# Kernel optimization log

Hardware: AMD Instinct MI355X
Metric: run time of the kernel (lower is better)

Reference implementation:

```python
import jax, jax.numpy as jnp
import numpy as np

B, S, OBS, NINS, H, NBLK = 1024, 512, 5, 2, 32, 4
EPS = 1e-6


def setup_inputs() -> dict:
    key = jax.random.key(0)
    ks = jax.random.split(key, 10)
    obs_sequence = jax.random.normal(ks[0], (B, S, OBS), jnp.float32)
    prev_actions = jax.random.normal(ks[1], (B, S, NINS), jnp.float32)
    fan_in = OBS + NINS
    # xavier-uniform input projection
    lim_in = np.sqrt(6.0 / (fan_in + H))
    W_in = jax.random.uniform(ks[2], (H, fan_in), jnp.float32, -lim_in, lim_in)
    b_in = jnp.zeros((H,), jnp.float32)
    rms_w = jnp.ones((NBLK, H), jnp.float32)
    # LSTMCell default init: U(-1/sqrt(H), 1/sqrt(H)); gate order i,f,g,o
    s = 1.0 / np.sqrt(H)
    W_ih = jax.random.uniform(ks[3], (NBLK, 4 * H, H), jnp.float32, -s, s)
    W_hh = jax.random.uniform(ks[4], (NBLK, 4 * H, H), jnp.float32, -s, s)
    b_ih = jax.random.uniform(ks[5], (NBLK, 4 * H), jnp.float32, -s, s)
    b_hh = jax.random.uniform(ks[6], (NBLK, 4 * H), jnp.float32, -s, s)
    # heads: kaiming-uniform (linear, fan_in) scaled by 1e-3, zero bias
    lim_h = np.sqrt(3.0 / H)
    head_w = jax.random.uniform(ks[7], (NINS, H), jnp.float32, -lim_h, lim_h) * 1e-3
    head_b = jnp.zeros((NINS,), jnp.float32)
    return dict(obs_sequence=obs_sequence, prev_actions=prev_actions,
                W_in=W_in, b_in=b_in, rms_w=rms_w,
                W_ih=W_ih, W_hh=W_hh, b_ih=b_ih, b_hh=b_hh,
                head_w=head_w, head_b=head_b)


def reference(obs_sequence, prev_actions, W_in, b_in, rms_w,
              W_ih, W_hh, b_ih, b_hh, head_w, head_b):
    batch = obs_sequence.shape[0]
    hdim = W_in.shape[0]
    x = jnp.concatenate([obs_sequence, prev_actions], axis=-1) @ W_in.T + b_in  # [B,S,H]
    xs = jnp.swapaxes(x, 0, 1)  # [S,B,H] for scan over time
    h0 = jnp.zeros((NBLK, batch, hdim), x.dtype)
    c0 = jnp.zeros((NBLK, batch, hdim), x.dtype)

    def step(carry, xt):
        h, c = carry
        hs, cs = [], []
        for k in range(NBLK):  # small fixed stack of distinct blocks
            rms = jnp.sqrt(jnp.mean(xt * xt, axis=-1, keepdims=True) + EPS)
            xn = rms_w[k] * (xt / rms)
            gates = xn @ W_ih[k].T + b_ih[k] + h[k] @ W_hh[k].T + b_hh[k]  # [B,4H]
            i, f, g, o = jnp.split(gates, 4, axis=-1)
            c_new = jax.nn.sigmoid(f) * c[k] + jax.nn.sigmoid(i) * jnp.tanh(g)
            h_new = jax.nn.sigmoid(o) * jnp.tanh(c_new)
            xt = xt + h_new  # residual
            hs.append(h_new)
            cs.append(c_new)
        return (jnp.stack(hs), jnp.stack(cs)), xt

    (hT, cT), ys = jax.lax.scan(step, (h0, c0), xs)  # ys: [S,B,H]
    raw = jnp.einsum('sbh,ih->ibs', ys, head_w) + head_b[:, None, None]  # [NINS,B,S]
    out = jnp.sign(raw) * (jnp.exp(jnp.abs(raw)) - 1.0)  # symexp
    lim = jnp.array([5.0, 10.0], out.dtype)[:, None, None]
    out = jnp.clip(out, -lim, lim)
    return out, hT, cT
```

## Files before the change

kernel.cpp:

```cpp
#include <hip/hip_runtime.h>


constexpr int B_ = 1024, S_ = 512, OBS_ = 5, NINS_ = 2, H_ = 32, NBLK_ = 4;
constexpr int SUP_ = 4;
constexpr int TT_ = S_ / SUP_;
constexpr float EPS_ = 1e-6f;
constexpr float LOG2E_ = 1.4426950408889634f;

typedef __fp16 h2 __attribute__((ext_vector_type(2)));
typedef __fp16 h8 __attribute__((ext_vector_type(8)));
typedef float  f4 __attribute__((ext_vector_type(4)));
typedef int    i4 __attribute__((ext_vector_type(4)));

__device__ __forceinline__ float rcp_(float x) { return __builtin_amdgcn_rcpf(x); }
__device__ __forceinline__ float rsq_(float x) { return __builtin_amdgcn_rsqf(x); }
__device__ __forceinline__ float ex2_(float x) { return __builtin_amdgcn_exp2f(x); }
__device__ __forceinline__ h2 pk_(float a, float b) {
  return __builtin_amdgcn_cvt_pkrtz(a, b);
}
__device__ __forceinline__ h8 pk8_(f4 lo, f4 hi) {
  i4 q;
  q[0] = __builtin_bit_cast(int, pk_(lo[0], lo[1]));
  q[1] = __builtin_bit_cast(int, pk_(lo[2], lo[3]));
  q[2] = __builtin_bit_cast(int, pk_(hi[0], hi[1]));
  q[3] = __builtin_bit_cast(int, pk_(hi[2], hi[3]));
  return __builtin_bit_cast(h8, q);
}
__device__ __forceinline__ f4 mfma_(h8 a, h8 b, f4 c) {
  return __builtin_amdgcn_mfma_f32_16x16x32_f16(a, b, c, 0, 0, 0);
}
__device__ __forceinline__ f4 e4n_(f4 a) {
  f4 r;
  r[0] = ex2_(-a[0]); r[1] = ex2_(-a[1]);
  r[2] = ex2_(-a[2]); r[3] = ex2_(-a[3]);
  return r;
}
__device__ __forceinline__ f4 rcp4_(f4 a) {
  f4 r;
  r[0] = rcp_(a[0]); r[1] = rcp_(a[1]);
  r[2] = rcp_(a[2]); r[3] = rcp_(a[3]);
  return r;
}
__device__ __forceinline__ float dot44_(f4 a, f4 x, f4 b2, f4 y) {
  float s = a[0] * x[0];
  s = fmaf(a[1], x[1], s); s = fmaf(a[2], x[2], s); s = fmaf(a[3], x[3], s);
  s = fmaf(b2[0], y[0], s); s = fmaf(b2[1], y[1], s);
  s = fmaf(b2[2], y[2], s); s = fmaf(b2[3], y[3], s);
  return s;
}
__device__ __forceinline__ float psw16_(float v, bool re) {
#if __has_builtin(__builtin_amdgcn_permlane16_swap)
  auto r = __builtin_amdgcn_permlane16_swap(
      __builtin_bit_cast(int, v), __builtin_bit_cast(int, v), false, false);
  return __builtin_bit_cast(float, re ? (int)r[1] : (int)r[0]);
#else
  return __shfl_xor(v, 16);
#endif
}
__device__ __forceinline__ float psw32_(float v, bool lo) {
#if __has_builtin(__builtin_amdgcn_permlane32_swap)
  auto r = __builtin_amdgcn_permlane32_swap(
      __builtin_bit_cast(int, v), __builtin_bit_cast(int, v), false, false);
  return __builtin_bit_cast(float, lo ? (int)r[1] : (int)r[0]);
#else
  return __shfl_xor(v, 32);
#endif
}

#define ACT_TILE(GI, GF, GG, GO, C, HV) do {                               \
    const f4 _one = {1.f, 1.f, 1.f, 1.f};                                  \
    const f4 _Ei = e4n_(GI);                                               \
    const f4 _Eg = e4n_(GG);                                               \
    const f4 _Ef = e4n_(GF);                                               \
    const f4 _sitg = (_one - _Eg) * rcp4_((_one + _Ei) * (_one + _Eg));    \
    const f4 _sf = rcp4_(_one + _Ef);                                      \
    (C) = _sf * (C) + _sitg;                                               \
    const f4 _Eo = e4n_(GO);                                               \
    const f4 _Ec = e4n_((C) * (2.f * LOG2E_));                             \
    (HV) = (_one - _Ec) * rcp4_((_one + _Eo) * (_one + _Ec));              \
  } while (0)

__global__ __launch_bounds__(256, 1) void garch_mfma7_kernel(
    const float* __restrict__ obs, const float* __restrict__ prev,
    const float* __restrict__ W_in, const float* __restrict__ b_in,
    const float* __restrict__ rms_w,
    const float* __restrict__ W_ih, const float* __restrict__ W_hh,
    const float* __restrict__ b_ih, const float* __restrict__ b_hh,
    const float* __restrict__ head_w, const float* __restrict__ head_b,
    float* __restrict__ out) {
  const int tid  = threadIdx.x;
  const int k    = tid >> 6;
  const int lane = tid & 63;
  const int g    = lane >> 4;
  const int b    = lane & 15;
  const int bg   = blockIdx.x * 16 + b;
  const bool re_ = ((lane >> 4) & 1) == 0;
  const bool lo_ = (lane < 32);

  __shared__ __align__(16) float xslot[3][2][SUP_][16][36];

  h8 wx[8], wh[8];
  f4 biasv[8];
  {
    const size_t wb = (size_t)k * 128 * 32;
#pragma unroll
    for (int mi = 0; mi < 8; ++mi) {
      const float scl = (mi == 4 || mi == 5) ? 2.f * LOG2E_ : LOG2E_;
      const int row = 16 * mi + b;
      const float* px = W_ih + wb + (size_t)row * 32;
      f4 x0 = *(const f4*)(px + 4 * g);
      f4 x1 = *(const f4*)(px + 16 + 4 * g);
      wx[mi] = pk8_(x0 * scl, x1 * scl);
      const float* ph = W_hh + wb + (size_t)row * 32;
      f4 h0v = *(const f4*)(ph + 4 * g);
      f4 h1v = *(const f4*)(ph + 16 + 4 * g);
      wh[mi] = pk8_(h0v * scl, h1v * scl);
      f4 bv;
#pragma unroll
      for (int r = 0; r < 4; ++r) {
        const int gr = k * 128 + 16 * mi + 4 * g + r;
        bv[r] = (b_ih[gr] + b_hh[gr]) * scl;
      }
      biasv[mi] = bv;
    }
  }
  f4 rw0v, rw1v;
#pragma unroll
  for (int r = 0; r < 4; ++r) {
    rw0v[r] = rms_w[k * 32 + 4 * g + r];
    rw1v[r] = rms_w[k * 32 + 16 + 4 * g + r];
  }

  h8 winA0 = {}, winA1 = {};
  f4 bin0v = {}, bin1v = {};
  const float* obs_b = nullptr; const float* prev_b = nullptr;
  f4 cin[SUP_] = {}, nin[SUP_] = {};
  if (k == 0) {
    f4 lo0, lo1; const f4 z = {};
#pragma unroll
    for (int r = 0; r < 4; ++r) {
      const int kk = 4 * g + r;
      lo0[r] = (kk < 7) ? W_in[(size_t)b * 7 + kk] : 0.f;
      lo1[r] = (kk < 7) ? W_in[(size_t)(16 + b) * 7 + kk] : 0.f;
    }
    winA0 = pk8_(lo0, z);
    winA1 = pk8_(lo1, z);
#pragma unroll
    for (int r = 0; r < 4; ++r) {
      bin0v[r] = b_in[4 * g + r];
      bin1v[r] = b_in[16 + 4 * g + r];
    }
    obs_b  = obs  + (size_t)bg * S_ * OBS_;
    prev_b = prev + (size_t)bg * S_ * NINS_;
#pragma unroll
    for (int s = 0; s < SUP_; ++s) {
      const float* o = obs_b + (size_t)s * OBS_;
      if (g == 0)      { cin[s][0] = o[0]; cin[s][1] = o[1]; cin[s][2] = o[2]; cin[s][3] = o[3]; }
      else if (g == 1) { cin[s][0] = o[4]; cin[s][1] = prev_b[2 * s]; cin[s][2] = prev_b[2 * s + 1]; cin[s][3] = 0.f; }
    }
  }
  f4 hw00 = {}, hw01 = {}, hw10 = {}, hw11 = {};
  float hb0 = 0.f, hb1 = 0.f;
  if (k == 3) {
#pragma unroll
    for (int r = 0; r < 4; ++r) {
      hw00[r] = head_w[4 * g + r]      * LOG2E_;
      hw01[r] = head_w[16 + 4 * g + r] * LOG2E_;
      hw10[r] = head_w[32 + 4 * g + r] * LOG2E_;
      hw11[r] = head_w[48 + 4 * g + r] * LOG2E_;
    }
    hb0 = head_b[0] * LOG2E_;
    hb1 = head_b[1] * LOG2E_;
  }

  f4 c0 = {}, c1 = {}, hv0 = {}, hv1 = {};

  float* out_y  = out;
  float* out_hT = out + (size_t)NINS_ * B_ * S_;
  float* out_cT = out_hT + (size_t)NBLK_ * B_ * H_;

  for (int tau = 0; tau < TT_ + NBLK_ - 1; ++tau) {
    __syncthreads();
    const int tt = tau - k;
    if (tt < 0 || tt >= TT_) continue;
    const int t0 = SUP_ * tt;
    const int wp = tau & 1, rp = (tau + 1) & 1;

    f4 x0[SUP_], x1[SUP_];
    if (k == 0) {
      if (tt + 1 < TT_) {
#pragma unroll
        for (int s = 0; s < SUP_; ++s) {
          const int t = t0 + SUP_ + s;
          const float* o = obs_b + (size_t)t * OBS_;
          if (g == 0)      { nin[s][0] = o[0]; nin[s][1] = o[1]; nin[s][2] = o[2]; nin[s][3] = o[3]; }
          else if (g == 1) { nin[s][0] = o[4]; nin[s][1] = prev_b[2 * t]; nin[s][2] = prev_b[2 * t + 1]; nin[s][3] = 0.f; }
        }
      }
      const f4 z = {};
#pragma unroll
      for (int s = 0; s < SUP_; ++s) {
        const h8 binp = pk8_(cin[s], z);
        x0[s] = mfma_(winA0, binp, bin0v);
        x1[s] = mfma_(winA1, binp, bin1v);
      }
    } else {
#pragma unroll
      for (int s = 0; s < SUP_; ++s) {
        x0[s] = *(const f4*)&xslot[k - 1][rp][s][b][4 * g];
        x1[s] = *(const f4*)&xslot[k - 1][rp][s][b][16 + 4 * g];
      }
    }

    h8 bx[SUP_];
#pragma unroll
    for (int s = 0; s < SUP_; ++s) {
      float ss = dot44_(x0[s], x0[s], x1[s], x1[s]);
      ss += psw16_(ss, re_);
      ss += psw32_(ss, lo_);
      const float rinv = rsq_(ss * (1.0f / 32.0f) + EPS_);
      bx[s] = pk8_(x0[s] * (rw0v * rinv), x1[s] * (rw1v * rinv));
    }
    f4 gx[SUP_][8];
#pragma unroll
    for (int s = 0; s < SUP_; ++s) {
#pragma unroll
      for (int m = 0; m < 8; ++m) {
        gx[s][m] = mfma_(wx[m], bx[s], biasv[m]);
      }
    }

#pragma unroll
    for (int s = 0; s < SUP_; ++s) {
      const h8 bh = pk8_(hv0, hv1);
      const f4 gi0 = mfma_(wh[0], bh, gx[s][0]);
      const f4 gi1 = mfma_(wh[1], bh, gx[s][1]);
      const f4 gf0 = mfma_(wh[2], bh, gx[s][2]);
      const f4 gf1 = mfma_(wh[3], bh, gx[s][3]);
      const f4 gg0 = mfma_(wh[4], bh, gx[s][4]);
      const f4 gg1 = mfma_(wh[5], bh, gx[s][5]);
      const f4 go0 = mfma_(wh[6], bh, gx[s][6]);
      const f4 go1 = mfma_(wh[7], bh, gx[s][7]);
      ACT_TILE(gi0, gf0, gg0, go0, c0, hv0);
      ACT_TILE(gi1, gf1, gg1, go1, c1, hv1);
      x0[s] += hv0;
      x1[s] += hv1;
    }

    if (k < 3) {
#pragma unroll
      for (int s = 0; s < SUP_; ++s) {
        *(f4*)&xslot[k][wp][s][b][4 * g]      = x0[s];
        *(f4*)&xslot[k][wp][s][b][16 + 4 * g] = x1[s];
      }
    } else {
      float p0[SUP_], p1[SUP_];
#pragma unroll
      for (int s = 0; s < SUP_; ++s) {
        float a = dot44_(hw00, x0[s], hw01, x1[s]);
        float bq = dot44_(hw10, x0[s], hw11, x1[s]);
        a += psw16_(a, re_); a += psw32_(a, lo_);
        bq += psw16_(bq, re_); bq += psw32_(bq, lo_);
        p0[s] = a + hb0;
        p1[s] = bq + hb1;
      }
      if (lane < 16) {
        f4 v0, v1;
#pragma unroll
        for (int s = 0; s < SUP_; ++s) {
          v0[s] = copysignf(fminf(ex2_(fabsf(p0[s])) - 1.f, 5.f),  p0[s]);
          v1[s] = copysignf(fminf(ex2_(fabsf(p1[s])) - 1.f, 10.f), p1[s]);
        }
        *(f4*)&out_y[(size_t)bg * S_ + t0]                   = v0;
        *(f4*)&out_y[(size_t)B_ * S_ + (size_t)bg * S_ + t0] = v1;
      }
    }

    if (tt == TT_ - 1) {
      float* hp = out_hT + ((size_t)k * B_ + bg) * H_;
      float* cp = out_cT + ((size_t)k * B_ + bg) * H_;
#pragma unroll
      for (int r = 0; r < 4; ++r) {
        hp[4 * g + r]      = hv0[r];
        hp[16 + 4 * g + r] = hv1[r];
        cp[4 * g + r]      = c0[r];
        cp[16 + 4 * g + r] = c1[r];
      }
    }

    if (k == 0) {
#pragma unroll
      for (int s = 0; s < SUP_; ++s) cin[s] = nin[s];
    }
  }
}

extern "C" void kernel_launch(void* const* d_in, const int* in_sizes, int n_in,
                              void* d_out, int out_size, void* d_ws, size_t ws_size,
                              hipStream_t stream) {
  (void)in_sizes; (void)n_in; (void)d_ws; (void)ws_size; (void)out_size;
  garch_mfma7_kernel<<<dim3(B_ / 16), dim3(256), 0, stream>>>(
      (const float*)d_in[0],
      (const float*)d_in[1],
      (const float*)d_in[2],
      (const float*)d_in[3],
      (const float*)d_in[4],
      (const float*)d_in[5],
      (const float*)d_in[6],
      (const float*)d_in[7],
      (const float*)d_in[8],
      (const float*)d_in[9],
      (const float*)d_in[10],
      (float*)d_out);
}
```

Before: 429.4 us.

## Double timesteps per barrier stage and merge LSTM sigmoid reciprocals

```diff
diff --git a/kernel.cpp b/kernel.cpp
--- a/kernel.cpp
+++ b/kernel.cpp
@@ -2,7 +2,8 @@
 
 
 constexpr int B_ = 1024, S_ = 512, OBS_ = 5, NINS_ = 2, H_ = 32, NBLK_ = 4;
-constexpr int SUP_ = 4;
+constexpr int SUP_ = 8;
+constexpr int PH_  = 4;
 constexpr int TT_ = S_ / SUP_;
 constexpr float EPS_ = 1e-6f;
 constexpr float LOG2E_ = 1.4426950408889634f;
@@ -72,15 +73,18 @@
     const f4 _Ei = e4n_(GI);                                               \
     const f4 _Eg = e4n_(GG);                                               \
     const f4 _Ef = e4n_(GF);                                               \
-    const f4 _sitg = (_one - _Eg) * rcp4_((_one + _Ei) * (_one + _Eg));    \
-    const f4 _sf = rcp4_(_one + _Ef);                                      \
+    const f4 _a = (_one + _Ei) * (_one + _Eg);                             \
+    const f4 _f = _one + _Ef;                                              \
+    const f4 _r = rcp4_(_a * _f);                                          \
+    const f4 _sitg = (_one - _Eg) * _f * _r;                               \
+    const f4 _sf = _a * _r;                                                \
     (C) = _sf * (C) + _sitg;                                               \
     const f4 _Eo = e4n_(GO);                                               \
     const f4 _Ec = e4n_((C) * (2.f * LOG2E_));                             \
     (HV) = (_one - _Ec) * rcp4_((_one + _Eo) * (_one + _Ec));              \
   } while (0)
 
-__global__ __launch_bounds__(256, 1) void garch_mfma7_kernel(
+__global__ __launch_bounds__(256, 1) void garch_mfma8_kernel(
     const float* __restrict__ obs, const float* __restrict__ prev,
     const float* __restrict__ W_in, const float* __restrict__ b_in,
     const float* __restrict__ rms_w,
@@ -134,7 +138,7 @@
   h8 winA0 = {}, winA1 = {};
   f4 bin0v = {}, bin1v = {};
   const float* obs_b = nullptr; const float* prev_b = nullptr;
-  f4 cin[SUP_] = {}, nin[SUP_] = {};
+  f4 cin[SUP_] = {};
   if (k == 0) {
     f4 lo0, lo1; const f4 z = {};
 #pragma unroll
@@ -186,93 +190,100 @@
     const int t0 = SUP_ * tt;
     const int wp = tau & 1, rp = (tau + 1) & 1;
 
-    f4 x0[SUP_], x1[SUP_];
-    if (k == 0) {
-      if (tt + 1 < TT_) {
-#pragma unroll
-        for (int s = 0; s < SUP_; ++s) {
-          const int t = t0 + SUP_ + s;
-          const float* o = obs_b + (size_t)t * OBS_;
-          if (g == 0)      { nin[s][0] = o[0]; nin[s][1] = o[1]; nin[s][2] = o[2]; nin[s][3] = o[3]; }
-          else if (g == 1) { nin[s][0] = o[4]; nin[s][1] = prev_b[2 * t]; nin[s][2] = prev_b[2 * t + 1]; nin[s][3] = 0.f; }
-        }
-      }
-      const f4 z = {};
-#pragma unroll
-      for (int s = 0; s < SUP_; ++s) {
-        const h8 binp = pk8_(cin[s], z);
-        x0[s] = mfma_(winA0, binp, bin0v);
-        x1[s] = mfma_(winA1, binp, bin1v);
-      }
-    } else {
-#pragma unroll
-      for (int s = 0; s < SUP_; ++s) {
-        x0[s] = *(const f4*)&xslot[k - 1][rp][s][b][4 * g];
-        x1[s] = *(const f4*)&xslot[k - 1][rp][s][b][16 + 4 * g];
-      }
-    }
-
-    h8 bx[SUP_];
-#pragma unroll
-    for (int s = 0; s < SUP_; ++s) {
-      float ss = dot44_(x0[s], x0[s], x1[s], x1[s]);
-      ss += psw16_(ss, re_);
-      ss += psw32_(ss, lo_);
-      const float rinv = rsq_(ss * (1.0f / 32.0f) + EPS_);
-      bx[s] = pk8_(x0[s] * (rw0v * rinv), x1[s] * (rw1v * rinv));
-    }
-    f4 gx[SUP_][8];
-#pragma unroll
-    for (int s = 0; s < SUP_; ++s) {
-#pragma unroll
-      for (int m = 0; m < 8; ++m) {
-        gx[s][m] = mfma_(wx[m], bx[s], biasv[m]);
-      }
-    }
-
-#pragma unroll
-    for (int s = 0; s < SUP_; ++s) {
-      const h8 bh = pk8_(hv0, hv1);
-      const f4 gi0 = mfma_(wh[0], bh, gx[s][0]);
-      const f4 gi1 = mfma_(wh[1], bh, gx[s][1]);
-      const f4 gf0 = mfma_(wh[2], bh, gx[s][2]);
-      const f4 gf1 = mfma_(wh[3], bh, gx[s][3]);
-      const f4 gg0 = mfma_(wh[4], bh, gx[s][4]);
-      const f4 gg1 = mfma_(wh[5], bh, gx[s][5]);
-      const f4 go0 = mfma_(wh[6], bh, gx[s][6]);
-      const f4 go1 = mfma_(wh[7], bh, gx[s][7]);
-      ACT_TILE(gi0, gf0, gg0, go0, c0, hv0);
-      ACT_TILE(gi1, gf1, gg1, go1, c1, hv1);
-      x0[s] += hv0;
-      x1[s] += hv1;
-    }
-
-    if (k < 3) {
-#pragma unroll
-      for (int s = 0; s < SUP_; ++s) {
-        *(f4*)&xslot[k][wp][s][b][4 * g]      = x0[s];
-        *(f4*)&xslot[k][wp][s][b][16 + 4 * g] = x1[s];
-      }
-    } else {
-      float p0[SUP_], p1[SUP_];
-#pragma unroll
-      for (int s = 0; s < SUP_; ++s) {
-        float a = dot44_(hw00, x0[s], hw01, x1[s]);
-        float bq = dot44_(hw10, x0[s], hw11, x1[s]);
-        a += psw16_(a, re_); a += psw32_(a, lo_);
-        bq += psw16_(bq, re_); bq += psw32_(bq, lo_);
-        p0[s] = a + hb0;
-        p1[s] = bq + hb1;
-      }
-      if (lane < 16) {
-        f4 v0, v1;
-#pragma unroll
-        for (int s = 0; s < SUP_; ++s) {
-          v0[s] = copysignf(fminf(ex2_(fabsf(p0[s])) - 1.f, 5.f),  p0[s]);
-          v1[s] = copysignf(fminf(ex2_(fabsf(p1[s])) - 1.f, 10.f), p1[s]);
-        }
-        *(f4*)&out_y[(size_t)bg * S_ + t0]                   = v0;
-        *(f4*)&out_y[(size_t)B_ * S_ + (size_t)bg * S_ + t0] = v1;
+#pragma unroll
+    for (int p = 0; p < SUP_ / PH_; ++p) {
+      f4 x0[PH_], x1[PH_];
+      if (k == 0) {
+        const f4 z = {};
+#pragma unroll
+        for (int s = 0; s < PH_; ++s) {
+          const int sg_ = p * PH_ + s;
+          const h8 binp = pk8_(cin[sg_], z);
+          x0[s] = mfma_(winA0, binp, bin0v);
+          x1[s] = mfma_(winA1, binp, bin1v);
+        }
+        if (tt + 1 < TT_) {
+#pragma unroll
+          for (int s = 0; s < PH_; ++s) {
+            const int sg_ = p * PH_ + s;
+            const int t = t0 + SUP_ + sg_;
+            const float* o = obs_b + (size_t)t * OBS_;
+            if (g == 0)      { cin[sg_][0] = o[0]; cin[sg_][1] = o[1]; cin[sg_][2] = o[2]; cin[sg_][3] = o[3]; }
+            else if (g == 1) { cin[sg_][0] = o[4]; cin[sg_][1] = prev_b[2 * t]; cin[sg_][2] = prev_b[2 * t + 1]; cin[sg_][3] = 0.f; }
+          }
+        }
+      } else {
+#pragma unroll
+        for (int s = 0; s < PH_; ++s) {
+          const int sg_ = p * PH_ + s;
+          x0[s] = *(const f4*)&xslot[k - 1][rp][sg_][b][4 * g];
+          x1[s] = *(const f4*)&xslot[k - 1][rp][sg_][b][16 + 4 * g];
+        }
+      }
+
+      h8 bx[PH_];
+#pragma unroll
+      for (int s = 0; s < PH_; ++s) {
+        float ss = dot44_(x0[s], x0[s], x1[s], x1[s]);
+        ss += psw16_(ss, re_);
+        ss += psw32_(ss, lo_);
+        const float rinv = rsq_(ss * (1.0f / 32.0f) + EPS_);
+        bx[s] = pk8_(x0[s] * (rw0v * rinv), x1[s] * (rw1v * rinv));
+      }
+      f4 gx[PH_][8];
+#pragma unroll
+      for (int s = 0; s < PH_; ++s) {
+#pragma unroll
+        for (int m = 0; m < 8; ++m) {
+          gx[s][m] = mfma_(wx[m], bx[s], biasv[m]);
+        }
+      }
+
+#pragma unroll
+      for (int s = 0; s < PH_; ++s) {
+        const h8 bh = pk8_(hv0, hv1);
+        const f4 gi0 = mfma_(wh[0], bh, gx[s][0]);
+        const f4 gi1 = mfma_(wh[1], bh, gx[s][1]);
+        const f4 gf0 = mfma_(wh[2], bh, gx[s][2]);
+        const f4 gf1 = mfma_(wh[3], bh, gx[s][3]);
+        const f4 gg0 = mfma_(wh[4], bh, gx[s][4]);
+        const f4 gg1 = mfma_(wh[5], bh, gx[s][5]);
+        const f4 go0 = mfma_(wh[6], bh, gx[s][6]);
+        const f4 go1 = mfma_(wh[7], bh, gx[s][7]);
+        ACT_TILE(gi0, gf0, gg0, go0, c0, hv0);
+        ACT_TILE(gi1, gf1, gg1, go1, c1, hv1);
+        x0[s] += hv0;
+        x1[s] += hv1;
+      }
+
+      if (k < 3) {
+#pragma unroll
+        for (int s = 0; s < PH_; ++s) {
+          const int sg_ = p * PH_ + s;
+          *(f4*)&xslot[k][wp][sg_][b][4 * g]      = x0[s];
+          *(f4*)&xslot[k][wp][sg_][b][16 + 4 * g] = x1[s];
+        }
+      } else {
+        float p0[PH_], p1[PH_];
+#pragma unroll
+        for (int s = 0; s < PH_; ++s) {
+          float a = dot44_(hw00, x0[s], hw01, x1[s]);
+          float bq = dot44_(hw10, x0[s], hw11, x1[s]);
+          a += psw16_(a, re_); a += psw32_(a, lo_);
+          bq += psw16_(bq, re_); bq += psw32_(bq, lo_);
+          p0[s] = a + hb0;
+          p1[s] = bq + hb1;
+        }
+        if (lane < 16) {
+          f4 v0, v1;
+#pragma unroll
+          for (int s = 0; s < PH_; ++s) {
+            v0[s] = copysignf(fminf(ex2_(fabsf(p0[s])) - 1.f, 5.f),  p0[s]);
+            v1[s] = copysignf(fminf(ex2_(fabsf(p1[s])) - 1.f, 10.f), p1[s]);
+          }
+          *(f4*)&out_y[(size_t)bg * S_ + t0 + p * PH_]                   = v0;
+          *(f4*)&out_y[(size_t)B_ * S_ + (size_t)bg * S_ + t0 + p * PH_] = v1;
+        }
       }
     }
 
@@ -287,11 +298,6 @@
         cp[16 + 4 * g + r] = c1[r];
       }
     }
-
-    if (k == 0) {
-#pragma unroll
-      for (int s = 0; s < SUP_; ++s) cin[s] = nin[s];
-    }
   }
 }
 
@@ -299,7 +305,7 @@
                               void* d_out, int out_size, void* d_ws, size_t ws_size,
                               hipStream_t stream) {
   (void)in_sizes; (void)n_in; (void)d_ws; (void)ws_size; (void)out_size;
-  garch_mfma7_kernel<<<dim3(B_ / 16), dim3(256), 0, stream>>>(
+  garch_mfma8_kernel<<<dim3(B_ / 16), dim3(256), 0, stream>>>(
       (const float*)d_in[0],
       (const float*)d_in[1],
       (const float*)d_in[2],
```

Result: no change. 425.7 us, median of 2 (-0.9%).

## Split each LSTM block across two waves with LDS flag handoff per step

Applied to the files above, without the earlier changes.

```diff
diff --git a/kernel.cpp b/kernel.cpp
--- a/kernel.cpp
+++ b/kernel.cpp
@@ -41,11 +41,11 @@
   r[2] = rcp_(a[2]); r[3] = rcp_(a[3]);
   return r;
 }
-__device__ __forceinline__ float dot44_(f4 a, f4 x, f4 b2, f4 y) {
+__device__ __forceinline__ float dot4_(f4 a, f4 x) {
   float s = a[0] * x[0];
-  s = fmaf(a[1], x[1], s); s = fmaf(a[2], x[2], s); s = fmaf(a[3], x[3], s);
-  s = fmaf(b2[0], y[0], s); s = fmaf(b2[1], y[1], s);
-  s = fmaf(b2[2], y[2], s); s = fmaf(b2[3], y[3], s);
+  s = fmaf(a[1], x[1], s);
+  s = fmaf(a[2], x[2], s);
+  s = fmaf(a[3], x[3], s);
   return s;
 }
 __device__ __forceinline__ float psw16_(float v, bool re) {
@@ -66,21 +66,32 @@
   return __shfl_xor(v, 32);
 #endif
 }
-
-#define ACT_TILE(GI, GF, GG, GO, C, HV) do {                               \
+__device__ __forceinline__ void flag_st_(int* p, int v) {
+  __threadfence_block();
+  __hip_atomic_store(p, v, __ATOMIC_RELAXED, __HIP_MEMORY_SCOPE_WORKGROUP);
+}
+__device__ __forceinline__ void flag_wait_(int* p, int v) {
+  while (__hip_atomic_load(p, __ATOMIC_RELAXED, __HIP_MEMORY_SCOPE_WORKGROUP) < v) {}
+  __threadfence_block();
+}
+
+#define ACT1(GI, GF, GG, GO) do {                                          \
     const f4 _one = {1.f, 1.f, 1.f, 1.f};                                  \
     const f4 _Ei = e4n_(GI);                                               \
     const f4 _Eg = e4n_(GG);                                               \
     const f4 _Ef = e4n_(GF);                                               \
-    const f4 _sitg = (_one - _Eg) * rcp4_((_one + _Ei) * (_one + _Eg));    \
-    const f4 _sf = rcp4_(_one + _Ef);                                      \
-    (C) = _sf * (C) + _sitg;                                               \
+    const f4 _a = (_one + _Ei) * (_one + _Eg);                             \
+    const f4 _f = _one + _Ef;                                              \
+    const f4 _r = rcp4_(_a * _f);                                          \
+    const f4 _sitg = (_one - _Eg) * _f * _r;                               \
+    const f4 _sf = _a * _r;                                                \
+    c_own = _sf * c_own + _sitg;                                           \
     const f4 _Eo = e4n_(GO);                                               \
-    const f4 _Ec = e4n_((C) * (2.f * LOG2E_));                             \
-    (HV) = (_one - _Ec) * rcp4_((_one + _Eo) * (_one + _Ec));              \
+    const f4 _Ec = e4n_(c_own * (2.f * LOG2E_));                           \
+    hv_own = (_one - _Ec) * rcp4_((_one + _Eo) * (_one + _Ec));            \
   } while (0)
 
-__global__ __launch_bounds__(256, 1) void garch_mfma7_kernel(
+__global__ __launch_bounds__(512, 1) void garch_msplit2_kernel(
     const float* __restrict__ obs, const float* __restrict__ prev,
     const float* __restrict__ W_in, const float* __restrict__ b_in,
     const float* __restrict__ rms_w,
@@ -89,7 +100,9 @@
     const float* __restrict__ head_w, const float* __restrict__ head_b,
     float* __restrict__ out) {
   const int tid  = threadIdx.x;
-  const int k    = tid >> 6;
+  const int w    = tid >> 6;
+  const int k    = w & 3;
+  const int hf   = w >> 2;
   const int lane = tid & 63;
   const int g    = lane >> 4;
   const int b    = lane & 15;
@@ -98,58 +111,62 @@
   const bool lo_ = (lane < 32);
 
   __shared__ __align__(16) float xslot[3][2][SUP_][16][36];
-
-  h8 wx[8], wh[8];
-  f4 biasv[8];
+  __shared__ int   xnbuf[4][2][SUP_][64][2];
+  __shared__ int   hvbuf[4][2][2][64][2];
+  __shared__ float ssbuf[4][2][SUP_][16];
+  __shared__ float headbuf[2][SUP_][16];
+  __shared__ int   xnflag[4][2];
+  __shared__ int   hvflag[4][2];
+  __shared__ int   headflag;
+
+  for (int i = tid; i < 4 * 2 * 2 * 64 * 2; i += 512) ((int*)hvbuf)[i] = 0;
+  if (tid < 8) { xnflag[tid >> 1][tid & 1] = 0; hvflag[tid >> 1][tid & 1] = 0; }
+  if (tid == 8) headflag = 0;
+
+  h8 wx[4], wh[4];
+  f4 biasv[4];
   {
     const size_t wb = (size_t)k * 128 * 32;
 #pragma unroll
-    for (int mi = 0; mi < 8; ++mi) {
-      const float scl = (mi == 4 || mi == 5) ? 2.f * LOG2E_ : LOG2E_;
-      const int row = 16 * mi + b;
+    for (int l = 0; l < 4; ++l) {
+      const int m = 2 * l + hf;
+      const float scl = (l == 2) ? 2.f * LOG2E_ : LOG2E_;
+      const int row = 16 * m + b;
       const float* px = W_ih + wb + (size_t)row * 32;
       f4 x0 = *(const f4*)(px + 4 * g);
       f4 x1 = *(const f4*)(px + 16 + 4 * g);
-      wx[mi] = pk8_(x0 * scl, x1 * scl);
+      wx[l] = pk8_(x0 * scl, x1 * scl);
       const float* ph = W_hh + wb + (size_t)row * 32;
       f4 h0v = *(const f4*)(ph + 4 * g);
       f4 h1v = *(const f4*)(ph + 16 + 4 * g);
-      wh[mi] = pk8_(h0v * scl, h1v * scl);
+      wh[l] = pk8_(h0v * scl, h1v * scl);
       f4 bv;
 #pragma unroll
       for (int r = 0; r < 4; ++r) {
-        const int gr = k * 128 + 16 * mi + 4 * g + r;
+        const int gr = k * 128 + 16 * m + 4 * g + r;
         bv[r] = (b_ih[gr] + b_hh[gr]) * scl;
       }
-      biasv[mi] = bv;
+      biasv[l] = bv;
     }
   }
-  f4 rw0v, rw1v;
-#pragma unroll
-  for (int r = 0; r < 4; ++r) {
-    rw0v[r] = rms_w[k * 32 + 4 * g + r];
-    rw1v[r] = rms_w[k * 32 + 16 + 4 * g + r];
-  }
-
-  h8 winA0 = {}, winA1 = {};
-  f4 bin0v = {}, bin1v = {};
+  f4 rwv;
+#pragma unroll
+  for (int r = 0; r < 4; ++r) rwv[r] = rms_w[k * 32 + 16 * hf + 4 * g + r];
+
+  h8 win = {};
+  f4 binv = {};
   const float* obs_b = nullptr; const float* prev_b = nullptr;
   f4 cin[SUP_] = {}, nin[SUP_] = {};
   if (k == 0) {
-    f4 lo0, lo1; const f4 z = {};
+    f4 lw; const f4 z = {};
 #pragma unroll
     for (int r = 0; r < 4; ++r) {
       const int kk = 4 * g + r;
-      lo0[r] = (kk < 7) ? W_in[(size_t)b * 7 + kk] : 0.f;
-      lo1[r] = (kk < 7) ? W_in[(size_t)(16 + b) * 7 + kk] : 0.f;
-    }
-    winA0 = pk8_(lo0, z);
-    winA1 = pk8_(lo1, z);
-#pragma unroll
-    for (int r = 0; r < 4; ++r) {
-      bin0v[r] = b_in[4 * g + r];
-      bin1v[r] = b_in[16 + 4 * g + r];
-    }
+      lw[r] = (kk < 7) ? W_in[(size_t)(16 * hf + b) * 7 + kk] : 0.f;
+    }
+    win = pk8_(lw, z);
+#pragma unroll
+    for (int r = 0; r < 4; ++r) binv[r] = b_in[16 * hf + 4 * g + r];
     obs_b  = obs  + (size_t)bg * S_ * OBS_;
     prev_b = prev + (size_t)bg * S_ * NINS_;
 #pragma unroll
@@ -159,21 +176,20 @@
       else if (g == 1) { cin[s][0] = o[4]; cin[s][1] = prev_b[2 * s]; cin[s][2] = prev_b[2 * s + 1]; cin[s][3] = 0.f; }
     }
   }
-  f4 hw00 = {}, hw01 = {}, hw10 = {}, hw11 = {};
+  f4 hwa = {}, hwb = {};
   float hb0 = 0.f, hb1 = 0.f;
   if (k == 3) {
 #pragma unroll
     for (int r = 0; r < 4; ++r) {
-      hw00[r] = head_w[4 * g + r]      * LOG2E_;
-      hw01[r] = head_w[16 + 4 * g + r] * LOG2E_;
-      hw10[r] = head_w[32 + 4 * g + r] * LOG2E_;
-      hw11[r] = head_w[48 + 4 * g + r] * LOG2E_;
+      hwa[r] = head_w[16 * hf + 4 * g + r]      * LOG2E_;
+      hwb[r] = head_w[32 + 16 * hf + 4 * g + r] * LOG2E_;
     }
     hb0 = head_b[0] * LOG2E_;
     hb1 = head_b[1] * LOG2E_;
   }
 
-  f4 c0 = {}, c1 = {}, hv0 = {}, hv1 = {};
+  f4 c_own = {}, hv_own = {};
+  int hvpk0 = 0, hvpk1 = 0;
 
   float* out_y  = out;
   float* out_hT = out + (size_t)NINS_ * B_ * S_;
@@ -186,7 +202,7 @@
     const int t0 = SUP_ * tt;
     const int wp = tau & 1, rp = (tau + 1) & 1;
 
-    f4 x0[SUP_], x1[SUP_];
+    f4 xt[SUP_];
     if (k == 0) {
       if (tt + 1 < TT_) {
 #pragma unroll
@@ -201,78 +217,113 @@
 #pragma unroll
       for (int s = 0; s < SUP_; ++s) {
         const h8 binp = pk8_(cin[s], z);
-        x0[s] = mfma_(winA0, binp, bin0v);
-        x1[s] = mfma_(winA1, binp, bin1v);
+        xt[s] = mfma_(win, binp, binv);
       }
     } else {
 #pragma unroll
-      for (int s = 0; s < SUP_; ++s) {
-        x0[s] = *(const f4*)&xslot[k - 1][rp][s][b][4 * g];
-        x1[s] = *(const f4*)&xslot[k - 1][rp][s][b][16 + 4 * g];
-      }
-    }
-
-    h8 bx[SUP_];
-#pragma unroll
-    for (int s = 0; s < SUP_; ++s) {
-      float ss = dot44_(x0[s], x0[s], x1[s], x1[s]);
+      for (int s = 0; s < SUP_; ++s)
+        xt[s] = *(const f4*)&xslot[k - 1][rp][s][b][16 * hf + 4 * g];
+    }
+
+    int xnp0[SUP_], xnp1[SUP_];
+    float ssp[SUP_];
+#pragma unroll
+    for (int s = 0; s < SUP_; ++s) {
+      const f4 xn = xt[s] * rwv;
+      xnp0[s] = __builtin_bit_cast(int, pk_(xn[0], xn[1]));
+      xnp1[s] = __builtin_bit_cast(int, pk_(xn[2], xn[3]));
+      float ss = dot4_(xt[s], xt[s]);
       ss += psw16_(ss, re_);
       ss += psw32_(ss, lo_);
-      const float rinv = rsq_(ss * (1.0f / 32.0f) + EPS_);
-      bx[s] = pk8_(x0[s] * (rw0v * rinv), x1[s] * (rw1v * rinv));
-    }
-    f4 gx[SUP_][8];
-#pragma unroll
-    for (int s = 0; s < SUP_; ++s) {
-#pragma unroll
-      for (int m = 0; m < 8; ++m) {
-        gx[s][m] = mfma_(wx[m], bx[s], biasv[m]);
-      }
-    }
-
-#pragma unroll
-    for (int s = 0; s < SUP_; ++s) {
-      const h8 bh = pk8_(hv0, hv1);
-      const f4 gi0 = mfma_(wh[0], bh, gx[s][0]);
-      const f4 gi1 = mfma_(wh[1], bh, gx[s][1]);
-      const f4 gf0 = mfma_(wh[2], bh, gx[s][2]);
-      const f4 gf1 = mfma_(wh[3], bh, gx[s][3]);
-      const f4 gg0 = mfma_(wh[4], bh, gx[s][4]);
-      const f4 gg1 = mfma_(wh[5], bh, gx[s][5]);
-      const f4 go0 = mfma_(wh[6], bh, gx[s][6]);
-      const f4 go1 = mfma_(wh[7], bh, gx[s][7]);
-      ACT_TILE(gi0, gf0, gg0, go0, c0, hv0);
-      ACT_TILE(gi1, gf1, gg1, go1, c1, hv1);
-      x0[s] += hv0;
-      x1[s] += hv1;
+      ssp[s] = ss;
+      int* p = &xnbuf[k][hf][s][lane][0];
+      p[0] = xnp0[s]; p[1] = xnp1[s];
+      if (lane < 16) ssbuf[k][hf][s][lane] = ss;
+    }
+    flag_st_(&xnflag[k][hf], tt + 1);
+    flag_wait_(&xnflag[k][hf ^ 1], tt + 1);
+
+    float rinv[SUP_];
+    h8 bx[SUP_];
+#pragma unroll
+    for (int s = 0; s < SUP_; ++s) {
+      const int* p = &xnbuf[k][hf ^ 1][s][lane][0];
+      const int o0 = p[0], o1 = p[1];
+      i4 q;
+      if (hf == 0) { q[0] = xnp0[s]; q[1] = xnp1[s]; q[2] = o0; q[3] = o1; }
+      else         { q[0] = o0; q[1] = o1; q[2] = xnp0[s]; q[3] = xnp1[s]; }
+      bx[s] = __builtin_bit_cast(h8, q);
+      const float ss = ssp[s] + ssbuf[k][hf ^ 1][s][b];
+      rinv[s] = rsq_(ss * (1.0f / 32.0f) + EPS_);
+    }
+    f4 gx[SUP_][4];
+    const f4 z4 = {};
+#pragma unroll
+    for (int s = 0; s < SUP_; ++s) {
+#pragma unroll
+      for (int l = 0; l < 4; ++l) gx[s][l] = mfma_(wx[l], bx[s], z4);
+    }
+
+#pragma unroll
+    for (int s = 0; s < SUP_; ++s) {
+      const int gs = tt * SUP_ + s + 1;
+      flag_wait_(&hvflag[k][hf ^ 1], gs - 1);
+      const int* hp = &hvbuf[k][hf ^ 1][(gs - 1) & 1][lane][0];
+      const int ho0 = hp[0], ho1 = hp[1];
+      i4 qh;
+      if (hf == 0) { qh[0] = hvpk0; qh[1] = hvpk1; qh[2] = ho0; qh[3] = ho1; }
+      else         { qh[0] = ho0; qh[1] = ho1; qh[2] = hvpk0; qh[3] = hvpk1; }
+      const h8 bh = __builtin_bit_cast(h8, qh);
+      const f4 g0 = gx[s][0] * rinv[s] + mfma_(wh[0], bh, biasv[0]);
+      const f4 g1 = gx[s][1] * rinv[s] + mfma_(wh[1], bh, biasv[1]);
+      const f4 g2 = gx[s][2] * rinv[s] + mfma_(wh[2], bh, biasv[2]);
+      const f4 g3 = gx[s][3] * rinv[s] + mfma_(wh[3], bh, biasv[3]);
+      ACT1(g0, g1, g2, g3);
+      xt[s] += hv_own;
+      hvpk0 = __builtin_bit_cast(int, pk_(hv_own[0], hv_own[1]));
+      hvpk1 = __builtin_bit_cast(int, pk_(hv_own[2], hv_own[3]));
+      int* hq = &hvbuf[k][hf][gs & 1][lane][0];
+      hq[0] = hvpk0; hq[1] = hvpk1;
+      flag_st_(&hvflag[k][hf], gs);
     }
 
     if (k < 3) {
 #pragma unroll
+      for (int s = 0; s < SUP_; ++s)
+        *(f4*)&xslot[k][wp][s][b][16 * hf + 4 * g] = xt[s];
+    } else {
+      float pa[SUP_], pb[SUP_];
+#pragma unroll
       for (int s = 0; s < SUP_; ++s) {
-        *(f4*)&xslot[k][wp][s][b][4 * g]      = x0[s];
-        *(f4*)&xslot[k][wp][s][b][16 + 4 * g] = x1[s];
-      }
-    } else {
-      float p0[SUP_], p1[SUP_];
-#pragma unroll
-      for (int s = 0; s < SUP_; ++s) {
-        float a = dot44_(hw00, x0[s], hw01, x1[s]);
-        float bq = dot44_(hw10, x0[s], hw11, x1[s]);
-        a += psw16_(a, re_); a += psw32_(a, lo_);
-        bq += psw16_(bq, re_); bq += psw32_(bq, lo_);
-        p0[s] = a + hb0;
-        p1[s] = bq + hb1;
-      }
-      if (lane < 16) {
-        f4 v0, v1;
-#pragma unroll
-        for (int s = 0; s < SUP_; ++s) {
-          v0[s] = copysignf(fminf(ex2_(fabsf(p0[s])) - 1.f, 5.f),  p0[s]);
-          v1[s] = copysignf(fminf(ex2_(fabsf(p1[s])) - 1.f, 10.f), p1[s]);
+        float a = dot4_(hwa, xt[s]);
+        float bb = dot4_(hwb, xt[s]);
+        a += psw16_(a, re_);  a += psw32_(a, lo_);
+        bb += psw16_(bb, re_); bb += psw32_(bb, lo_);
+        pa[s] = a; pb[s] = bb;
+      }
+      if (hf == 0) {
+        if (lane < 16) {
+#pragma unroll
+          for (int s = 0; s < SUP_; ++s) {
+            headbuf[0][s][lane] = pa[s];
+            headbuf[1][s][lane] = pb[s];
+          }
         }
-        *(f4*)&out_y[(size_t)bg * S_ + t0]                   = v0;
-        *(f4*)&out_y[(size_t)B_ * S_ + (size_t)bg * S_ + t0] = v1;
+        flag_st_(&headflag, tt + 1);
+      } else {
+        flag_wait_(&headflag, tt + 1);
+        if (lane < 16) {
+          f4 v0, v1;
+#pragma unroll
+          for (int s = 0; s < SUP_; ++s) {
+            const float p0 = pa[s] + headbuf[0][s][lane] + hb0;
+            const float p1 = pb[s] + headbuf[1][s][lane] + hb1;
+            v0[s] = copysignf(fminf(ex2_(fabsf(p0)) - 1.f, 5.f),  p0);
+            v1[s] = copysignf(fminf(ex2_(fabsf(p1)) - 1.f, 10.f), p1);
+          }
+          *(f4*)&out_y[(size_t)bg * S_ + t0]                   = v0;
+          *(f4*)&out_y[(size_t)B_ * S_ + (size_t)bg * S_ + t0] = v1;
+        }
       }
     }
 
@@ -281,10 +332,8 @@
       float* cp = out_cT + ((size_t)k * B_ + bg) * H_;
 #pragma unroll
       for (int r = 0; r < 4; ++r) {
-        hp[4 * g + r]      = hv0[r];
-        hp[16 + 4 * g + r] = hv1[r];
-        cp[4 * g + r]      = c0[r];
-        cp[16 + 4 * g + r] = c1[r];
+        hp[16 * hf + 4 * g + r] = hv_own[r];
+        cp[16 * hf + 4 * g + r] = c_own[r];
       }
     }
 
@@ -299,7 +348,7 @@
                               void* d_out, int out_size, void* d_ws, size_t ws_size,
                               hipStream_t stream) {
   (void)in_sizes; (void)n_in; (void)d_ws; (void)ws_size; (void)out_size;
-  garch_mfma7_kernel<<<dim3(B_ / 16), dim3(256), 0, stream>>>(
+  garch_msplit2_kernel<<<dim3(B_ / 16), dim3(512), 0, stream>>>(
       (const float*)d_in[0],
       (const float*)d_in[1],
       (const float*)d_in[2],
```

New measurement: 508.1 us. 18.3% more time.
